# Performance work log

Hardware: AMD Instinct MI355X
Metric: run time of the kernel (lower is better)

Reference implementation:

```python
import jax, jax.numpy as jnp
import numpy as np

B, NX, NC, D, H = 4, 1024, 154, 1536, 24
HD = D // H
MH = int(D * 4.0)
EPS = 1e-6


def setup_inputs() -> dict:
    key = jax.random.key(0)
    ks = jax.random.split(key, 20)
    s = lambda i, shape, fan: jax.random.normal(ks[i], shape, jnp.float32) * (1.0 / np.sqrt(fan))
    return {
        "x": jax.random.normal(ks[0], (B, NX, D), jnp.float32),
        "c": jax.random.normal(ks[1], (B, NC, D), jnp.float32),
        "vec": jax.random.normal(ks[2], (B, D), jnp.float32),
        "w_mod": s(3, (D, 6 * D), D), "b_mod": jnp.zeros((6 * D,), jnp.float32),
        "w_qkv_x": s(4, (D, 3 * D), D), "b_qkv_x": jnp.zeros((3 * D,), jnp.float32),
        "w_qkv_c": s(5, (D, 3 * D), D), "b_qkv_c": jnp.zeros((3 * D,), jnp.float32),
        "w_proj_x": s(6, (D, D), D), "b_proj_x": jnp.zeros((D,), jnp.float32),
        "w_proj_c": s(7, (D, D), D), "b_proj_c": jnp.zeros((D,), jnp.float32),
        "w1_x": s(8, (D, MH), D), "b1_x": jnp.zeros((MH,), jnp.float32),
        "w2_x": s(9, (MH, D), MH), "b2_x": jnp.zeros((D,), jnp.float32),
        "w1_c": s(10, (D, MH), D), "b1_c": jnp.zeros((MH,), jnp.float32),
        "w2_c": s(11, (MH, D), MH), "b2_c": jnp.zeros((D,), jnp.float32),
    }


def _ln(t):
    m = jnp.mean(t, axis=-1, keepdims=True)
    v = jnp.var(t, axis=-1, keepdims=True)
    return (t - m) * jax.lax.rsqrt(v + EPS)


def reference(x, c, vec, w_mod, b_mod, w_qkv_x, b_qkv_x, w_qkv_c, b_qkv_c,
              w_proj_x, b_proj_x, w_proj_c, b_proj_c,
              w1_x, b1_x, w2_x, b2_x, w1_c, b1_c, w2_c, b2_c):
    # adaLN modulation: silu(vec) @ W -> 6 chunks, each [B,1,D]
    mod = (jax.nn.silu(vec) @ w_mod + b_mod)[:, None, :]
    sh_x, sc_x, g_x, sh_c, sc_c, g_c = jnp.split(mod, 6, axis=2)

    x_n = _ln(x) * (1 + sc_x) + sh_x
    c_n = _ln(c) * (1 + sc_c) + sh_c

    def qkv(t, w, b, n):
        o = (t @ w + b).reshape(t.shape[0], n, 3, H, HD)
        return o[:, :, 0], o[:, :, 1], o[:, :, 2]  # each [B,N,H,HD]

    qx, kx, vx = qkv(x_n, w_qkv_x, b_qkv_x, NX)
    qc, kc, vc = qkv(c_n, w_qkv_c, b_qkv_c, NC)
    q = jnp.concatenate([qx, qc], axis=1)
    k = jnp.concatenate([kx, kc], axis=1)
    v = jnp.concatenate([vx, vc], axis=1)

    scale = HD ** -0.5
    attn = jnp.einsum("bshd,bthd->bhst", q, k) * scale
    attn = jax.nn.softmax(attn, axis=-1)
    o = jnp.einsum("bhst,bthd->bshd", attn, v).reshape(B, NX + NC, D)
    xo, co = o[:, :NX], o[:, NX:]

    x = x + g_x * (xo @ w_proj_x + b_proj_x)
    c = c + g_c * (co @ w_proj_c + b_proj_c)

    gelu = lambda t: jax.nn.gelu(t, approximate=True)
    x = x + (gelu(_ln(x) @ w1_x + b1_x) @ w2_x + b2_x)
    c = c + (gelu(_ln(c) @ w1_c + b1_c) @ w2_c + b2_c)
    return x, c
```

## Files before the change

kernel.cpp:

```cpp
#include <hip/hip_runtime.h>
#include <stdint.h>

typedef unsigned short u16;
typedef unsigned int u32;
typedef __attribute__((ext_vector_type(8))) short bf16x8;
typedef __attribute__((ext_vector_type(8))) unsigned short u16x8;
typedef __attribute__((ext_vector_type(2))) unsigned int u32x2;
typedef __attribute__((ext_vector_type(4))) float f32x4;

#define LB256 __launch_bounds__(256, 2)

#define BB 4
#define NX 1024
#define NC 154
#define NT 1178
#define NTP 1184
#define DD 1536
#define HH 24
#define MHD 6144
#define NQKV 4608
#define NMOD 9216
#define KSPL 6

__device__ __forceinline__ int imin(int a, int b) { return a < b ? a : b; }

__device__ __forceinline__ u16 f2bf(float f) {
  u32 u = __float_as_uint(f);
  u32 r = (u + 0x7fffu + ((u >> 16) & 1u)) >> 16;
  return (u16)r;
}

__device__ __forceinline__ float bf2f(u16 v) {
  u32 u = ((u32)v) << 16;
  return __uint_as_float(u);
}

__device__ __forceinline__ float gelu_t(float x) {
  float u = 1.5957691216f * x * fmaf(0.044715f, x * x, 1.f);
  return x / (1.f + __expf(-u));
}

__device__ __forceinline__ f32x4 fzero4() {
  f32x4 z; z[0] = 0.f; z[1] = 0.f; z[2] = 0.f; z[3] = 0.f; return z;
}

__device__ __forceinline__ void glds16(const u16* g, u16* l) {
  __builtin_amdgcn_global_load_lds(
      (const __attribute__((address_space(1))) void*)g,
      (__attribute__((address_space(3))) void*)l, 16, 0, 0);
}

#define WAITV4 asm volatile("s_waitcnt vmcnt(4)" ::: "memory")
#define WAITV0 asm volatile("s_waitcnt vmcnt(0)" ::: "memory")
#define SCHEDB __builtin_amdgcn_sched_barrier(0)

struct TDesc {
  const float* W[8];
  u16* Wt[8];
  int K[8];
  int N[8];
  int off[9];
};

__global__ void k_transpose8(TDesc d) {
  __shared__ float tile[32][33];
  int bid = blockIdx.x;
  int i = 0;
#pragma unroll
  for (int t = 1; t < 8; ++t)
    if (bid >= d.off[t]) i = t;
  const float* W = d.W[i];
  u16* Wt = d.Wt[i];
  const int K = d.K[i], N = d.N[i];
  const int local = bid - d.off[i];
  const int nbx = N >> 5;
  const int n0 = (local % nbx) * 32, k0 = (local / nbx) * 32;
  const int cx = threadIdx.x & 15, ry = threadIdx.x >> 4;
#pragma unroll
  for (int j = 0; j < 32; j += 16) {
    float2 t2 = *(const float2*)&W[(size_t)(k0 + ry + j) * N + n0 + cx * 2];
    tile[ry + j][cx * 2] = t2.x;
    tile[ry + j][cx * 2 + 1] = t2.y;
  }
  __syncthreads();
#pragma unroll
  for (int j = 0; j < 32; j += 16) {
    const int ny = ry + j;
    u32 w = (u32)f2bf(tile[cx * 2][ny]) | ((u32)f2bf(tile[cx * 2 + 1][ny]) << 16);
    *(u32*)&Wt[(size_t)(n0 + ny) * K + k0 + cx * 2] = w;
  }
}

__global__ void k_mod_part(const float* __restrict__ vec, const float* __restrict__ w_mod,
                           float* __restrict__ part) {
  __shared__ float sv[BB][256];
  int n = blockIdx.x * 256 + threadIdx.x;
  int kb = blockIdx.y;
  int k0 = kb * 256;
  for (int i = threadIdx.x; i < BB * 256; i += 256) {
    int b = i >> 8, kk = i & 255;
    float v = vec[b * DD + k0 + kk];
    sv[b][kk] = v / (1.f + __expf(-v));
  }
  __syncthreads();
  float a0 = 0.f, a1 = 0.f, a2 = 0.f, a3 = 0.f;
  for (int k = 0; k < 256; ++k) {
    float w = w_mod[(size_t)(k0 + k) * NMOD + n];
    a0 = fmaf(sv[0][k], w, a0);
    a1 = fmaf(sv[1][k], w, a1);
    a2 = fmaf(sv[2][k], w, a2);
    a3 = fmaf(sv[3][k], w, a3);
  }
  part[((size_t)kb * BB + 0) * NMOD + n] = a0;
  part[((size_t)kb * BB + 1) * NMOD + n] = a1;
  part[((size_t)kb * BB + 2) * NMOD + n] = a2;
  part[((size_t)kb * BB + 3) * NMOD + n] = a3;
}

__global__ void k_mod_red(const float* __restrict__ part, const float* __restrict__ b_mod,
                          float* __restrict__ mod) {
  int n = blockIdx.x * 256 + threadIdx.x;
  float bb = b_mod[n];
#pragma unroll
  for (int b = 0; b < BB; ++b) {
    float s = bb;
#pragma unroll
    for (int kb = 0; kb < KSPL; ++kb) s += part[((size_t)kb * BB + b) * NMOD + n];
    mod[b * NMOD + n] = s;
  }
}

__global__ LB256 void k_ln(const float* __restrict__ in, u16* __restrict__ out,
                           const float* __restrict__ modp, int sh_off, int sc_off,
                           int rows_per_b) {
  int row = blockIdx.x;
  int b = row / rows_per_b;
  const float2* xr = (const float2*)(in + (size_t)row * DD);
  float2 v[3];
  float s = 0.f, s2 = 0.f;
#pragma unroll
  for (int i = 0; i < 3; ++i) {
    float2 t = xr[threadIdx.x + 256 * i];
    v[i] = t;
    s += t.x + t.y;
    s2 += t.x * t.x + t.y * t.y;
  }
#pragma unroll
  for (int m = 32; m >= 1; m >>= 1) {
    s += __shfl_xor(s, m);
    s2 += __shfl_xor(s2, m);
  }
  __shared__ float red[8];
  int wid = threadIdx.x >> 6;
  if ((threadIdx.x & 63) == 0) { red[wid] = s; red[4 + wid] = s2; }
  __syncthreads();
  s = red[0] + red[1] + red[2] + red[3];
  s2 = red[4] + red[5] + red[6] + red[7];
  float mean = s * (1.f / (float)DD);
  float var = s2 * (1.f / (float)DD) - mean * mean;
  float rstd = rsqrtf(var + 1e-6f);
#pragma unroll
  for (int i = 0; i < 3; ++i) {
    int d = (threadIdx.x + 256 * i) * 2;
    float y0 = (v[i].x - mean) * rstd;
    float y1 = (v[i].y - mean) * rstd;
    if (modp) {
      float2 sc = *(const float2*)&modp[b * NMOD + sc_off + d];
      float2 sh = *(const float2*)&modp[b * NMOD + sh_off + d];
      y0 = y0 * (1.f + sc.x) + sh.x;
      y1 = y1 * (1.f + sc.y) + sh.y;
    }
    u32 w = (u32)f2bf(y0) | ((u32)f2bf(y1) << 16);
    *(u32*)&out[(size_t)row * DD + d] = w;
  }
}

template <int EPI>
__device__ __forceinline__ void gemm_epi(
    const f32x4 (&acc)[4][4], int m0, int n0, int wm, int wn, int g, int r,
    int M, int N, const float* bias, void* outp, const float* resid,
    const float* modp, int goff, int rpb, int zed,
    u16* qb, u16* kb, u16* vtb) {
#pragma unroll
  for (int mi = 0; mi < 4; ++mi) {
#pragma unroll
    for (int ni = 0; ni < 4; ++ni) {
      const int col = n0 + wn + ni * 16 + r;
      float bv = 0.f;
      if constexpr (EPI != 4) bv = bias[col];
#pragma unroll
      for (int j = 0; j < 4; ++j) {
        const int row = m0 + wm + mi * 16 + g * 4 + j;
        if (row >= M) continue;
        const size_t off = (size_t)row * N + col;
        float v = acc[mi][ni][j] + bv;
        if constexpr (EPI == 0) {
          ((u16*)outp)[off] = f2bf(v);
        } else if constexpr (EPI == 1) {
          ((u16*)outp)[off] = f2bf(gelu_t(v));
        } else if constexpr (EPI == 2) {
          const int b = row / rpb;
          ((float*)outp)[off] = resid[off] + modp[b * NMOD + goff + col] * v;
        } else if constexpr (EPI == 3) {
          ((float*)outp)[off] = resid[off] + v;
        } else if constexpr (EPI == 4) {
          ((u16*)outp)[(size_t)zed * (size_t)goff + off] = f2bf(acc[mi][ni][j]);
        } else {
          const int b = row / rpb;
          const int t = goff + (row - b * rpb);
          const u16 bw = f2bf(v);
          if (col < DD) {
            const int h = col >> 6, d = col & 63;
            qb[(((size_t)b * HH + h) * NT + t) * 64 + d] = bw;
          } else if (col < 2 * DD) {
            const int cc = col - DD;
            const int h = cc >> 6, d = cc & 63;
            kb[(((size_t)b * HH + h) * NT + t) * 64 + d] = bw;
          } else {
            const int cc = col - 2 * DD;
            const int h = cc >> 6, d = cc & 63;
            vtb[((size_t)b * HH + h) * (64 * NTP) + (size_t)d * NTP + t] = bw;
          }
        }
      }
    }
  }
}

template <int EPI1, int EPI2>
__global__ LB256 void k_gemm2(
    const u16* __restrict__ A1, const u16* __restrict__ Bt1, const float* __restrict__ bias1,
    int M1, int rpb1, int goff1, int kLen1,
    const u16* __restrict__ A2, const u16* __restrict__ Bt2, const float* __restrict__ bias2,
    int M2, int rpb2, int goff2, int kLen2,
    int yHi, int N, int lda, int ldb, int kzOff,
    void* __restrict__ out1, void* __restrict__ out2,
    const float* __restrict__ resid1, const float* __restrict__ resid2,
    const float* __restrict__ modp,
    u16* __restrict__ qb, u16* __restrict__ kb, u16* __restrict__ vtb) {
  __shared__ __align__(16) u16 sm[3 * 8192];
  const int tid = threadIdx.x;
  const int lane = tid & 63;
  const int g = lane >> 4, r = lane & 15;
  const int wid = tid >> 6;

  const int gx = gridDim.x;
  const int gyTot = gridDim.y;
  const int nwg = gx * gyTot;
  int wg = blockIdx.y * gx + blockIdx.x;
  {
    int q = nwg >> 3, rr = nwg & 7;
    int xcd = wg & 7, sl = wg >> 3;
    wg = (xcd < rr ? xcd * (q + 1) : rr * (q + 1) + (xcd - rr) * q) + sl;
  }
  int mIdx, nIdx;
  {
    const int np1 = (gx - 1) >> 3;
    const int lastw = gx - np1 * 8;
    const int full = gyTot * 8;
    if (wg < np1 * full) {
      int p = wg / full, off = wg % full;
      mIdx = off >> 3;
      nIdx = p * 8 + (off & 7);
    } else {
      int off = wg - np1 * full;
      mIdx = off / lastw;
      nIdx = np1 * 8 + off % lastw;
    }
  }
  const bool role2 = mIdx >= yHi;

  const u16* A = role2 ? A2 : A1;
  const u16* Bt = role2 ? Bt2 : Bt1;
  const int M = role2 ? M2 : M1;
  const int kLen = role2 ? kLen2 : kLen1;
  const int m0 = (role2 ? (mIdx - yHi) : mIdx) * 128, n0 = nIdx * 128;
  const int wm = (wid >> 1) * 64, wn = (wid & 1) * 64;
  A += (size_t)blockIdx.z * kzOff;
  Bt += (size_t)blockIdx.z * kzOff;

  f32x4 acc[4][4];
#pragma unroll
  for (int i = 0; i < 4; ++i)
#pragma unroll
    for (int j = 0; j < 4; ++j) acc[i][j] = fzero4();

  const int rl = lane >> 2;
  const int slg = (lane & 3) ^ ((lane >> 3) & 3);
  const int c0 = wid * 2, c1 = wid * 2 + 1;
  const size_t aR0 = (size_t)imin(m0 + c0 * 16 + rl, M - 1) * lda + slg * 8;
  const size_t aR1 = (size_t)imin(m0 + c1 * 16 + rl, M - 1) * lda + slg * 8;
  const size_t bR0 = (size_t)(n0 + c0 * 16 + rl) * ldb + slg * 8;
  const size_t bR1 = (size_t)(n0 + c1 * 16 + rl) * ldb + slg * 8;

  int aOff[4], bOff[4];
#pragma unroll
  for (int mi = 0; mi < 4; ++mi) aOff[mi] = (wm + mi * 16 + r) * 32 + ((g ^ ((r >> 1) & 3)) * 8);
#pragma unroll
  for (int ni = 0; ni < 4; ++ni) bOff[ni] = 4096 + (wn + ni * 16 + r) * 32 + ((g ^ ((r >> 1) & 3)) * 8);

  const int nt = kLen >> 5;

#define STAGE(BI, T)                                        \
  do {                                                      \
    u16* bb = &sm[(BI) * 8192];                             \
    size_t kk = (size_t)(T) * 32;                           \
    glds16(A + aR0 + kk, bb + c0 * 512);                    \
    glds16(A + aR1 + kk, bb + c1 * 512);                    \
    glds16(Bt + bR0 + kk, bb + 4096 + c0 * 512);            \
    glds16(Bt + bR1 + kk, bb + 4096 + c1 * 512);            \
  } while (0)

  STAGE(0, 0);
  STAGE(1, 1);

  for (int t = 0; t < nt - 1; ++t) {
    WAITV4;
    __builtin_amdgcn_s_barrier();
    SCHEDB;
    if (t + 2 < nt) STAGE((t + 2) % 3, t + 2);
    const u16* bb = &sm[(t % 3) * 8192];
    bf16x8 af[4], bfr[4];
#pragma unroll
    for (int mi = 0; mi < 4; ++mi) af[mi] = *(const bf16x8*)(bb + aOff[mi]);
#pragma unroll
    for (int ni = 0; ni < 4; ++ni) bfr[ni] = *(const bf16x8*)(bb + bOff[ni]);
    __builtin_amdgcn_s_setprio(1);
#pragma unroll
    for (int mi = 0; mi < 4; ++mi)
#pragma unroll
      for (int ni = 0; ni < 4; ++ni)
        acc[mi][ni] = __builtin_amdgcn_mfma_f32_16x16x32_bf16(af[mi], bfr[ni], acc[mi][ni], 0, 0, 0);
    __builtin_amdgcn_s_setprio(0);
    SCHEDB;
  }
  {
    WAITV0;
    __builtin_amdgcn_s_barrier();
    SCHEDB;
    const u16* bb = &sm[((nt - 1) % 3) * 8192];
    bf16x8 af[4], bfr[4];
#pragma unroll
    for (int mi = 0; mi < 4; ++mi) af[mi] = *(const bf16x8*)(bb + aOff[mi]);
#pragma unroll
    for (int ni = 0; ni < 4; ++ni) bfr[ni] = *(const bf16x8*)(bb + bOff[ni]);
#pragma unroll
    for (int mi = 0; mi < 4; ++mi)
#pragma unroll
      for (int ni = 0; ni < 4; ++ni)
        acc[mi][ni] = __builtin_amdgcn_mfma_f32_16x16x32_bf16(af[mi], bfr[ni], acc[mi][ni], 0, 0, 0);
  }
#undef STAGE

  if (role2)
    gemm_epi<EPI2>(acc, m0, n0, wm, wn, g, r, M, N, bias2, out2, resid2, modp,
                   goff2, rpb2, blockIdx.z, qb, kb, vtb);
  else
    gemm_epi<EPI1>(acc, m0, n0, wm, wn, g, r, M, N, bias1, out1, resid1, modp,
                   goff1, rpb1, blockIdx.z, qb, kb, vtb);
}

__global__ void k_red2(const u16* __restrict__ p0x, const u16* __restrict__ p1x,
                       const float* __restrict__ residx, const float* __restrict__ bx,
                       const u16* __restrict__ p0c, const u16* __restrict__ p1c,
                       const float* __restrict__ residc, const float* __restrict__ bc,
                       float* __restrict__ outx, float* __restrict__ outc) {
  int row = blockIdx.x;
  if (row < BB * NX) {
    size_t base = (size_t)row * DD;
#pragma unroll
    for (int i = 0; i < 6; ++i) {
      int j = threadIdx.x + 256 * i;
      outx[base + j] = residx[base + j] + bx[j] + bf2f(p0x[base + j]) + bf2f(p1x[base + j]);
    }
  } else {
    size_t base = (size_t)(row - BB * NX) * DD;
#pragma unroll
    for (int i = 0; i < 6; ++i) {
      int j = threadIdx.x + 256 * i;
      outc[base + j] = residc[base + j] + bc[j] + bf2f(p0c[base + j]) + bf2f(p1c[base + j]);
    }
  }
}

__global__ __launch_bounds__(512, 2) void k_attn(
    const u16* __restrict__ q, const u16* __restrict__ kk,
    const u16* __restrict__ vt, u16* __restrict__ ox, u16* __restrict__ oc) {
  __shared__ __align__(16) u16 Ks[64][72];
  __shared__ __align__(16) u16 Vs[64][72];
  __shared__ __align__(16) u16 Ps[8][16][72];

  const int lane = threadIdx.x & 63, wid = threadIdx.x >> 6;
  const int g = lane >> 4, r = lane & 15;
  const int q0 = blockIdx.x * 128;
  const int h = blockIdx.y, b = blockIdx.z;
  const size_t bh = (size_t)b * HH + h;
  const u16* qp = q + bh * (NT * 64);
  const u16* kp = kk + bh * (NT * 64);
  const u16* vp = vt + bh * (64 * NTP);

  const int qrow = imin(q0 + wid * 16 + r, NT - 1);
  u16x8 qr0 = *(const u16x8*)(qp + (size_t)qrow * 64 + g * 8);
  u16x8 qr1 = *(const u16x8*)(qp + (size_t)qrow * 64 + 32 + g * 8);
  bf16x8 qa0, qa1;
#pragma unroll
  for (int e = 0; e < 8; ++e) {
    qa0[e] = (short)f2bf(bf2f(qr0[e]) * 0.125f);
    qa1[e] = (short)f2bf(bf2f(qr1[e]) * 0.125f);
  }

  f32x4 oacc[4];
#pragma unroll
  for (int i = 0; i < 4; ++i) oacc[i] = fzero4();
  float mrow = -1e30f, lrow = 0.f;

  const int trA = threadIdx.x >> 3;
  const int ccA = (threadIdx.x & 7) * 8;

  u16x8 kreg, vreg;
#define LOADKV(T0)                                                     \
  do {                                                                 \
    int tsrc = imin((T0) + trA, NT - 1);                               \
    kreg = *(const u16x8*)(kp + (size_t)tsrc * 64 + ccA);              \
    int tcol = (T0) + ccA;                                             \
    if (tcol + 8 <= NT) {                                              \
      vreg = *(const u16x8*)(vp + (size_t)trA * NTP + tcol);           \
    } else {                                                           \
      _Pragma("unroll")                                                \
      for (int e = 0; e < 8; ++e)                                      \
        vreg[e] = vp[(size_t)trA * NTP + imin(tcol + e, NT - 1)];      \
    }                                                                  \
  } while (0)

  LOADKV(0);

  for (int t0 = 0; t0 < NT; t0 += 64) {
    if (t0) __syncthreads();
    *(u16x8*)&Ks[trA][ccA] = kreg;
    *(u16x8*)&Vs[trA][ccA] = vreg;
    __syncthreads();
    if (t0 + 64 < NT) LOADKV(t0 + 64);

    f32x4 s[4];
#pragma unroll
    for (int ni = 0; ni < 4; ++ni) {
      s[ni] = fzero4();
      s[ni] = __builtin_amdgcn_mfma_f32_16x16x32_bf16(*(const bf16x8*)&Ks[ni * 16 + r][g * 8], qa0, s[ni], 0, 0, 0);
      s[ni] = __builtin_amdgcn_mfma_f32_16x16x32_bf16(*(const bf16x8*)&Ks[ni * 16 + r][32 + g * 8], qa1, s[ni], 0, 0, 0);
    }

    float pv[4][4];
    float pm = -1e30f;
#pragma unroll
    for (int ni = 0; ni < 4; ++ni)
#pragma unroll
      for (int j = 0; j < 4; ++j) {
        int t = t0 + ni * 16 + g * 4 + j;
        float sv = (t < NT) ? s[ni][j] : -1e30f;
        pv[ni][j] = sv;
        pm = fmaxf(pm, sv);
      }
    pm = fmaxf(pm, __shfl_xor(pm, 16));
    pm = fmaxf(pm, __shfl_xor(pm, 32));

    float mn = fmaxf(mrow, pm);
    float alpha = __expf(mrow - mn);
    mrow = mn;
    float rs = 0.f;
#pragma unroll
    for (int ni = 0; ni < 4; ++ni)
#pragma unroll
      for (int j = 0; j < 4; ++j) {
        float p = __expf(pv[ni][j] - mn);
        pv[ni][j] = p;
        rs += p;
      }
    rs += __shfl_xor(rs, 16);
    rs += __shfl_xor(rs, 32);
    lrow = lrow * alpha + rs;

#pragma unroll
    for (int j = 0; j < 4; ++j) {
      float aj = __shfl(alpha, g * 4 + j);
#pragma unroll
      for (int ni = 0; ni < 4; ++ni) oacc[ni][j] *= aj;
    }

#pragma unroll
    for (int ni = 0; ni < 4; ++ni) {
      u32x2 w;
      w[0] = (u32)f2bf(pv[ni][0]) | ((u32)f2bf(pv[ni][1]) << 16);
      w[1] = (u32)f2bf(pv[ni][2]) | ((u32)f2bf(pv[ni][3]) << 16);
      *(u32x2*)&Ps[wid][r][ni * 16 + g * 4] = w;
    }

    bf16x8 pa0 = *(const bf16x8*)&Ps[wid][r][g * 8];
    bf16x8 pa1 = *(const bf16x8*)&Ps[wid][r][32 + g * 8];
#pragma unroll
    for (int ni = 0; ni < 4; ++ni) {
      oacc[ni] = __builtin_amdgcn_mfma_f32_16x16x32_bf16(pa0, *(const bf16x8*)&Vs[ni * 16 + r][g * 8], oacc[ni], 0, 0, 0);
      oacc[ni] = __builtin_amdgcn_mfma_f32_16x16x32_bf16(pa1, *(const bf16x8*)&Vs[ni * 16 + r][32 + g * 8], oacc[ni], 0, 0, 0);
    }
  }
#undef LOADKV

  float linv[4];
#pragma unroll
  for (int j = 0; j < 4; ++j) linv[j] = 1.f / __shfl(lrow, g * 4 + j);

#pragma unroll
  for (int ni = 0; ni < 4; ++ni)
#pragma unroll
    for (int j = 0; j < 4; ++j) {
      int tq = q0 + wid * 16 + g * 4 + j;
      if (tq >= NT) continue;
      float val = oacc[ni][j] * linv[j];
      int col = h * 64 + ni * 16 + r;
      if (tq < NX)
        ox[(size_t)(b * NX + tq) * DD + col] = f2bf(val);
      else
        oc[(size_t)(b * NC + tq - NX) * DD + col] = f2bf(val);
    }
}

extern "C" void kernel_launch(void* const* d_in, const int* in_sizes, int n_in,
                              void* d_out, int out_size, void* d_ws, size_t ws_size,
                              hipStream_t stream) {
  const float* x = (const float*)d_in[0];
  const float* c = (const float*)d_in[1];
  const float* vec = (const float*)d_in[2];
  const float* w_mod = (const float*)d_in[3];
  const float* b_mod = (const float*)d_in[4];
  const float* w_qkv_x = (const float*)d_in[5];
  const float* b_qkv_x = (const float*)d_in[6];
  const float* w_qkv_c = (const float*)d_in[7];
  const float* b_qkv_c = (const float*)d_in[8];
  const float* w_proj_x = (const float*)d_in[9];
  const float* b_proj_x = (const float*)d_in[10];
  const float* w_proj_c = (const float*)d_in[11];
  const float* b_proj_c = (const float*)d_in[12];
  const float* w1_x = (const float*)d_in[13];
  const float* b1_x = (const float*)d_in[14];
  const float* w2_x = (const float*)d_in[15];
  const float* b2_x = (const float*)d_in[16];
  const float* w1_c = (const float*)d_in[17];
  const float* b1_c = (const float*)d_in[18];
  const float* w2_c = (const float*)d_in[19];
  const float* b2_c = (const float*)d_in[20];

  if (ws_size < 229195776ull) return;

  char* ws = (char*)d_ws;
  u16* wt_qkv_x = (u16*)(ws + 0);
  u16* wt_qkv_c = (u16*)(ws + 14155776);
  u16* wt_proj_x = (u16*)(ws + 28311552);
  u16* wt_proj_c = (u16*)(ws + 33030144);
  u16* wt_w1_x = (u16*)(ws + 37748736);
  u16* wt_w1_c = (u16*)(ws + 56623104);
  u16* wt_w2_x = (u16*)(ws + 75497472);
  u16* wt_w2_c = (u16*)(ws + 94371840);
  float* modf = (float*)(ws + 113246208);
  char* S = ws + 113393664;
  u16* xn = (u16*)(S);
  u16* cn = (u16*)(S + 12582912);
  float* x2 = (float*)(S + 14475264);
  float* c2 = (float*)(S + 39641088);
  u16* pb0 = (u16*)(S);
  u16* pc0 = (u16*)(S + 12582912);
  u16* pb1 = (u16*)(S + 43425792);
  u16* pc1 = (u16*)(S + 56008704);
  const int PSTRIDE = 43425792 / 2;
  u16* qb = (u16*)(S + 57901056);
  u16* kb = (u16*)(S + 72376320);
  u16* vtb = (u16*)(S + 86851584);
  u16* hx = (u16*)(S + 57901056);
  u16* hc = (u16*)(S + 108232704);
  float* modpart = (float*)(S + 57901056);

  {
    TDesc d;
    const float* Ws[8] = {w_qkv_x, w_qkv_c, w_proj_x, w_proj_c, w1_x, w1_c, w2_x, w2_c};
    u16* Wts[8] = {wt_qkv_x, wt_qkv_c, wt_proj_x, wt_proj_c, wt_w1_x, wt_w1_c, wt_w2_x, wt_w2_c};
    int Ks[8] = {DD, DD, DD, DD, DD, DD, MHD, MHD};
    int Ns[8] = {NQKV, NQKV, DD, DD, MHD, MHD, DD, DD};
    int off = 0;
    for (int i = 0; i < 8; ++i) {
      d.W[i] = Ws[i]; d.Wt[i] = Wts[i]; d.K[i] = Ks[i]; d.N[i] = Ns[i];
      d.off[i] = off;
      off += (Ns[i] >> 5) * (Ks[i] >> 5);
    }
    d.off[8] = off;
    k_transpose8<<<dim3(off), 256, 0, stream>>>(d);
  }

  k_mod_part<<<dim3(NMOD / 256, KSPL), 256, 0, stream>>>(vec, w_mod, modpart);
  k_mod_red<<<dim3(NMOD / 256), 256, 0, stream>>>(modpart, b_mod, modf);

  k_ln<<<dim3(BB * NX), 256, 0, stream>>>(x, xn, modf, 0, DD, NX);
  k_ln<<<dim3(BB * NC), 256, 0, stream>>>(c, cn, modf, 3 * DD, 4 * DD, NC);

  k_gemm2<5, 5><<<dim3(NQKV / 128, 37), 256, 0, stream>>>(
      xn, wt_qkv_x, b_qkv_x, BB * NX, NX, 0, DD,
      cn, wt_qkv_c, b_qkv_c, BB * NC, NC, NX, DD,
      32, NQKV, DD, DD, 0, nullptr, nullptr, nullptr, nullptr, nullptr,
      qb, kb, vtb);

  k_attn<<<dim3((NT + 127) / 128, HH, BB), 512, 0, stream>>>(qb, kb, vtb, xn, cn);

  k_gemm2<2, 2><<<dim3(DD / 128, 37), 256, 0, stream>>>(
      xn, wt_proj_x, b_proj_x, BB * NX, NX, 2 * DD, DD,
      cn, wt_proj_c, b_proj_c, BB * NC, NC, 5 * DD, DD,
      32, DD, DD, DD, 0, x2, c2, x, c, modf, nullptr, nullptr, nullptr);

  k_ln<<<dim3(BB * NX), 256, 0, stream>>>(x2, xn, nullptr, 0, 0, NX);
  k_ln<<<dim3(BB * NC), 256, 0, stream>>>(c2, cn, nullptr, 0, 0, NC);

  k_gemm2<1, 1><<<dim3(MHD / 128, 37), 256, 0, stream>>>(
      xn, wt_w1_x, b1_x, BB * NX, NX, 0, DD,
      cn, wt_w1_c, b1_c, BB * NC, NC, 0, DD,
      32, MHD, DD, DD, 0, hx, hc, nullptr, nullptr, nullptr, nullptr, nullptr, nullptr);

  float* outx = (float*)d_out;
  float* outc = outx + (size_t)BB * NX * DD;
  k_gemm2<4, 4><<<dim3(DD / 128, 37, 2), 256, 0, stream>>>(
      hx, wt_w2_x, b2_x, BB * NX, NX, PSTRIDE, MHD / 2,
      hc, wt_w2_c, b2_c, BB * NC, NC, PSTRIDE, MHD / 2,
      32, DD, MHD, MHD, MHD / 2, pb0, pc0, nullptr, nullptr, nullptr,
      nullptr, nullptr, nullptr);
  k_red2<<<dim3(BB * (NX + NC)), 256, 0, stream>>>(
      pb0, pb1, x2, b2_x, pc0, pc1, c2, b2_c, outx, outc);
}
```

Measured before the change: 674.6 us.

## Switch GEMM to double-buffered BK=64 pipeline and merge x/c layernorm launches

The GEMM main loop moves from a 3-stage BK=32 pipeline with vmcnt(4) partial waits to a 2-stage BK=64 double buffer. Each iteration now waits for all loads, issues one barrier, and runs two 32-wide MFMA sub-steps. This halves the barrier count per K, but the wait is now a full drain, so less load latency is hidden behind compute. Separately, the paired x and c layernorm launches are merged into one k_ln2 kernel to cut two kernel launches.

Result: faster. 656.0 us (-2.8%).

```diff
diff --git a/kernel.cpp b/kernel.cpp
--- a/kernel.cpp
+++ b/kernel.cpp
@@ -50,7 +50,6 @@
       (__attribute__((address_space(3))) void*)l, 16, 0, 0);
 }
 
-#define WAITV4 asm volatile("s_waitcnt vmcnt(4)" ::: "memory")
 #define WAITV0 asm volatile("s_waitcnt vmcnt(0)" ::: "memory")
 #define SCHEDB __builtin_amdgcn_sched_barrier(0)
 
@@ -130,17 +129,30 @@
   }
 }
 
-__global__ LB256 void k_ln(const float* __restrict__ in, u16* __restrict__ out,
-                           const float* __restrict__ modp, int sh_off, int sc_off,
-                           int rows_per_b) {
+__global__ LB256 void k_ln2(const float* __restrict__ in1, u16* __restrict__ out1,
+                            const float* __restrict__ in2, u16* __restrict__ out2,
+                            const float* __restrict__ modp, int sh1, int sc1,
+                            int sh2, int sc2) {
   int row = blockIdx.x;
-  int b = row / rows_per_b;
-  const float2* xr = (const float2*)(in + (size_t)row * DD);
+  const float* xr;
+  u16* outp;
+  int b, sh, sc;
+  if (row < BB * NX) {
+    xr = in1 + (size_t)row * DD;
+    outp = out1 + (size_t)row * DD;
+    b = row / NX; sh = sh1; sc = sc1;
+  } else {
+    int r2 = row - BB * NX;
+    xr = in2 + (size_t)r2 * DD;
+    outp = out2 + (size_t)r2 * DD;
+    b = r2 / NC; sh = sh2; sc = sc2;
+  }
+  const float2* x2p = (const float2*)xr;
   float2 v[3];
   float s = 0.f, s2 = 0.f;
 #pragma unroll
   for (int i = 0; i < 3; ++i) {
-    float2 t = xr[threadIdx.x + 256 * i];
+    float2 t = x2p[threadIdx.x + 256 * i];
     v[i] = t;
     s += t.x + t.y;
     s2 += t.x * t.x + t.y * t.y;
@@ -165,13 +177,13 @@
     float y0 = (v[i].x - mean) * rstd;
     float y1 = (v[i].y - mean) * rstd;
     if (modp) {
-      float2 sc = *(const float2*)&modp[b * NMOD + sc_off + d];
-      float2 sh = *(const float2*)&modp[b * NMOD + sh_off + d];
-      y0 = y0 * (1.f + sc.x) + sh.x;
-      y1 = y1 * (1.f + sc.y) + sh.y;
+      float2 scv = *(const float2*)&modp[b * NMOD + sc + d];
+      float2 shv = *(const float2*)&modp[b * NMOD + sh + d];
+      y0 = y0 * (1.f + scv.x) + shv.x;
+      y1 = y1 * (1.f + scv.y) + shv.y;
     }
     u32 w = (u32)f2bf(y0) | ((u32)f2bf(y1) << 16);
-    *(u32*)&out[(size_t)row * DD + d] = w;
+    *(u32*)&outp[d] = w;
   }
 }
 
@@ -238,7 +250,7 @@
     const float* __restrict__ resid1, const float* __restrict__ resid2,
     const float* __restrict__ modp,
     u16* __restrict__ qb, u16* __restrict__ kb, u16* __restrict__ vtb) {
-  __shared__ __align__(16) u16 sm[3 * 8192];
+  __shared__ __align__(16) u16 sm[2 * 16384];
   const int tid = threadIdx.x;
   const int lane = tid & 63;
   const int g = lane >> 4, r = lane & 15;
@@ -299,58 +311,46 @@
 #pragma unroll
   for (int ni = 0; ni < 4; ++ni) bOff[ni] = 4096 + (wn + ni * 16 + r) * 32 + ((g ^ ((r >> 1) & 3)) * 8);
 
-  const int nt = kLen >> 5;
-
-#define STAGE(BI, T)                                        \
-  do {                                                      \
-    u16* bb = &sm[(BI) * 8192];                             \
-    size_t kk = (size_t)(T) * 32;                           \
-    glds16(A + aR0 + kk, bb + c0 * 512);                    \
-    glds16(A + aR1 + kk, bb + c1 * 512);                    \
-    glds16(Bt + bR0 + kk, bb + 4096 + c0 * 512);            \
-    glds16(Bt + bR1 + kk, bb + 4096 + c1 * 512);            \
+  const int nt = kLen >> 6;
+
+#define STAGE64(BI, T)                                          \
+  do {                                                          \
+    u16* bb = &sm[(BI) * 16384];                                \
+    _Pragma("unroll") for (int h = 0; h < 2; ++h) {             \
+      size_t kk = (size_t)(T) * 64 + h * 32;                    \
+      glds16(A + aR0 + kk, bb + h * 8192 + c0 * 512);           \
+      glds16(A + aR1 + kk, bb + h * 8192 + c1 * 512);           \
+      glds16(Bt + bR0 + kk, bb + h * 8192 + 4096 + c0 * 512);   \
+      glds16(Bt + bR1 + kk, bb + h * 8192 + 4096 + c1 * 512);   \
+    }                                                           \
   } while (0)
 
-  STAGE(0, 0);
-  STAGE(1, 1);
-
-  for (int t = 0; t < nt - 1; ++t) {
-    WAITV4;
-    __builtin_amdgcn_s_barrier();
-    SCHEDB;
-    if (t + 2 < nt) STAGE((t + 2) % 3, t + 2);
-    const u16* bb = &sm[(t % 3) * 8192];
-    bf16x8 af[4], bfr[4];
-#pragma unroll
-    for (int mi = 0; mi < 4; ++mi) af[mi] = *(const bf16x8*)(bb + aOff[mi]);
-#pragma unroll
-    for (int ni = 0; ni < 4; ++ni) bfr[ni] = *(const bf16x8*)(bb + bOff[ni]);
-    __builtin_amdgcn_s_setprio(1);
-#pragma unroll
-    for (int mi = 0; mi < 4; ++mi)
-#pragma unroll
-      for (int ni = 0; ni < 4; ++ni)
-        acc[mi][ni] = __builtin_amdgcn_mfma_f32_16x16x32_bf16(af[mi], bfr[ni], acc[mi][ni], 0, 0, 0);
-    __builtin_amdgcn_s_setprio(0);
-    SCHEDB;
-  }
-  {
+  STAGE64(0, 0);
+
+  for (int t = 0; t < nt; ++t) {
     WAITV0;
     __builtin_amdgcn_s_barrier();
     SCHEDB;
-    const u16* bb = &sm[((nt - 1) % 3) * 8192];
-    bf16x8 af[4], bfr[4];
-#pragma unroll
-    for (int mi = 0; mi < 4; ++mi) af[mi] = *(const bf16x8*)(bb + aOff[mi]);
-#pragma unroll
-    for (int ni = 0; ni < 4; ++ni) bfr[ni] = *(const bf16x8*)(bb + bOff[ni]);
-#pragma unroll
-    for (int mi = 0; mi < 4; ++mi)
-#pragma unroll
-      for (int ni = 0; ni < 4; ++ni)
-        acc[mi][ni] = __builtin_amdgcn_mfma_f32_16x16x32_bf16(af[mi], bfr[ni], acc[mi][ni], 0, 0, 0);
-  }
-#undef STAGE
+    if (t + 1 < nt) STAGE64((t + 1) & 1, t + 1);
+    const u16* bb = &sm[(t & 1) * 16384];
+#pragma unroll
+    for (int h = 0; h < 2; ++h) {
+      bf16x8 af[4], bfr[4];
+#pragma unroll
+      for (int mi = 0; mi < 4; ++mi) af[mi] = *(const bf16x8*)(bb + h * 8192 + aOff[mi]);
+#pragma unroll
+      for (int ni = 0; ni < 4; ++ni) bfr[ni] = *(const bf16x8*)(bb + h * 8192 + bOff[ni]);
+      __builtin_amdgcn_s_setprio(1);
+#pragma unroll
+      for (int mi = 0; mi < 4; ++mi)
+#pragma unroll
+        for (int ni = 0; ni < 4; ++ni)
+          acc[mi][ni] = __builtin_amdgcn_mfma_f32_16x16x32_bf16(af[mi], bfr[ni], acc[mi][ni], 0, 0, 0);
+      __builtin_amdgcn_s_setprio(0);
+    }
+    SCHEDB;
+  }
+#undef STAGE64
 
   if (role2)
     gemm_epi<EPI2>(acc, m0, n0, wm, wn, g, r, M, N, bias2, out2, resid2, modp,
@@ -596,8 +596,7 @@
   k_mod_part<<<dim3(NMOD / 256, KSPL), 256, 0, stream>>>(vec, w_mod, modpart);
   k_mod_red<<<dim3(NMOD / 256), 256, 0, stream>>>(modpart, b_mod, modf);
 
-  k_ln<<<dim3(BB * NX), 256, 0, stream>>>(x, xn, modf, 0, DD, NX);
-  k_ln<<<dim3(BB * NC), 256, 0, stream>>>(c, cn, modf, 3 * DD, 4 * DD, NC);
+  k_ln2<<<dim3(BB * (NX + NC)), 256, 0, stream>>>(x, xn, c, cn, modf, 0, DD, 3 * DD, 4 * DD);
 
   k_gemm2<5, 5><<<dim3(NQKV / 128, 37), 256, 0, stream>>>(
       xn, wt_qkv_x, b_qkv_x, BB * NX, NX, 0, DD,
@@ -612,8 +611,7 @@
       cn, wt_proj_c, b_proj_c, BB * NC, NC, 5 * DD, DD,
       32, DD, DD, DD, 0, x2, c2, x, c, modf, nullptr, nullptr, nullptr);
 
-  k_ln<<<dim3(BB * NX), 256, 0, stream>>>(x2, xn, nullptr, 0, 0, NX);
-  k_ln<<<dim3(BB * NC), 256, 0, stream>>>(c2, cn, nullptr, 0, 0, NC);
+  k_ln2<<<dim3(BB * (NX + NC)), 256, 0, stream>>>(x2, xn, c2, cn, nullptr, 0, 0, 0, 0);
 
   k_gemm2<1, 1><<<dim3(MHD / 128, 37), 256, 0, stream>>>(
       xn, wt_w1_x, b1_x, BB * NX, NX, 0, DD,
```
